# Optimization experiments

Measured on AMD Instinct MI355X. Metric: run time of the kernel, lower is better.

## Reference

```python
import jax, jax.numpy as jnp
import numpy as np
from jax import lax

B, T, U, V = 8, 160, 80, 512
BLANK = 0
FASTEMIT_LAMBDA = 0.0


def setup_inputs() -> dict:
    key = jax.random.key(0)
    k1, k2, k3, k4 = jax.random.split(key, 4)
    acts = jax.random.normal(k1, (B, T, U + 1, V), dtype=jnp.float32)
    labels = jax.random.randint(k2, (B, U), 1, V, dtype=jnp.int32)
    act_lens = jax.random.randint(k3, (B,), T // 2, T + 1, dtype=jnp.int32)
    label_lens = jax.random.randint(k4, (B,), U // 2, U + 1, dtype=jnp.int32)
    return {"acts": acts, "labels": labels, "act_lens": act_lens, "label_lens": label_lens}


def _alpha(blank_lp, label_lp):
    """Forward DP over the (T, U+1) lattice for one sample.
    blank_lp: [T, U+1] log P(blank | t, u);  label_lp: [T, U] log P(y_{u+1} | t, u).
    alpha[t, u] = logaddexp(alpha[t-1, u] + blank_lp[t-1, u], alpha[t, u-1] + label_lp[t, u-1]).
    """
    # row t=0: only label emissions -> prefix sums
    row0 = jnp.concatenate([jnp.zeros((1,), blank_lp.dtype), jnp.cumsum(label_lp[0])])

    def t_step(prev_row, xs):
        blank_prev, lab = xs                 # blank_lp[t-1]: [U+1], label_lp[t]: [U]
        base = prev_row + blank_prev         # come-from-below term, all u

        def u_step(carry, bl):
            b, l = bl
            new = jnp.logaddexp(b, carry + l)  # come-from-left recurrence along u
            return new, new

        _, rest = lax.scan(u_step, base[0], (base[1:], lab))
        row = jnp.concatenate([base[:1], rest])
        return row, row

    _, rows = lax.scan(t_step, row0, (blank_lp[:-1], label_lp[1:]))
    return jnp.concatenate([row0[None], rows], axis=0)  # [T, U+1]


def _rnnt_loss(acts, labels, act_lens, label_lens, blank=BLANK, fastemit_lambda=FASTEMIT_LAMBDA):
    lp = jax.nn.log_softmax(acts, axis=-1)                 # [B, T, U+1, V]
    blank_lp = lp[..., blank]                              # [B, T, U+1]
    # gather log-prob of emitting labels[u] at grid cell (t, u), u < U
    label_lp = jnp.take_along_axis(lp[:, :, :-1, :], labels[:, None, :, None], axis=-1)[..., 0]  # [B, T, U]
    alpha = jax.vmap(_alpha)(blank_lp, label_lp)           # [B, T, U+1]
    b_idx = jnp.arange(acts.shape[0])
    t_idx = act_lens - 1
    ll = alpha[b_idx, t_idx, label_lens] + blank_lp[b_idx, t_idx, label_lens]
    return -(1.0 + fastemit_lambda) * ll                   # [B]


def reference(acts, labels, act_lens, label_lens):
    return _rnnt_loss(acts, labels, act_lens, label_lens)
```

## Files before the change

kernel.cpp:

```cpp
#include <hip/hip_runtime.h>
#include <math.h>

#define RB 8
#define RT 160
#define RU 80
#define RV 512
#define UP1 81

#define L2E  1.44269504f
#define LN2  0.69314718f
#define NEGB (-1e30f)

__device__ __forceinline__ float fexp2(float x) { return __builtin_amdgcn_exp2f(x); }
__device__ __forceinline__ float flog2(float x) { return __builtin_amdgcn_logf(x); }

__device__ __forceinline__ float laE(float a, float b) {
    float m = fmaxf(a, b);
    float d = fminf(a, b) - m;
    return m + LN2 * flog2(1.0f + fexp2(d * L2E));
}

template<int CTRL, int RM>
__device__ __forceinline__ float dppf(float oldv, float src) {
    return __int_as_float(__builtin_amdgcn_update_dpp(
        __float_as_int(oldv), __float_as_int(src), CTRL, RM, 0xF, false));
}

__global__ __launch_bounds__(256) void lse_kernel(
    const float* __restrict__ acts, const int* __restrict__ labels,
    float* __restrict__ blank_lp, float* __restrict__ label_lp)
{
    const int wave = threadIdx.x >> 6;
    const int lane = threadIdx.x & 63;
    const int cell = blockIdx.x * 4 + wave;

    const int b   = cell / (RT * UP1);
    const int rem = cell - b * (RT * UP1);
    const int t   = rem / UP1;
    const int u   = rem - t * UP1;

    const float* p = acts + (size_t)cell * RV + lane * 8;
    const float4 v0 = *(const float4*)p;
    const float4 v1 = *(const float4*)(p + 4);

    float s = ((fexp2(v0.x * L2E) + fexp2(v0.y * L2E))
             + (fexp2(v0.z * L2E) + fexp2(v0.w * L2E)))
            + ((fexp2(v1.x * L2E) + fexp2(v1.y * L2E))
             + (fexp2(v1.z * L2E) + fexp2(v1.w * L2E)));

    s += dppf<0xB1,  0xF>(0.f, s);
    s += dppf<0x4E,  0xF>(0.f, s);
    s += dppf<0x141, 0xF>(0.f, s);
    s += dppf<0x140, 0xF>(0.f, s);
    s += dppf<0x142, 0xA>(0.f, s);
    s += dppf<0x143, 0xC>(0.f, s);

    const float lse = flog2(s) * LN2;
    const float blank_logit =
        __int_as_float(__builtin_amdgcn_readlane(__float_as_int(v0.x), 0));

    if (lane == 63) blank_lp[(b * RT + t) * UP1 + u] = blank_logit - lse;
    if (lane == 62 && u < RU) {
        const int lab = labels[b * RU + u];
        label_lp[(b * RT + t) * RU + u] = acts[(size_t)cell * RV + lab] - lse;
    }
}

__global__ __launch_bounds__(64) void dp_kernel(
    const float* __restrict__ blank_lp,
    const float* __restrict__ label_lp,
    const int* __restrict__ act_lens, const int* __restrict__ label_lens,
    float* __restrict__ out)
{
    const int b    = blockIdx.x;
    const int lane = threadIdx.x;
    const int u0   = lane * 2;
    const int u1   = lane * 2 + 1;
    const bool val0 = (u0 <= RU);
    const bool val1 = (u1 <= RU);

    const int t_idx = act_lens[b] - 1;
    const int ulen  = label_lens[b];

    const float* Bb = blank_lp + (size_t)b * RT * UP1;
    const float* Lb = label_lp + (size_t)b * RT * RU;

    float res  = 0.0f;
    bool  have = false;

    auto scanrow = [&](float b0_, float l0_, float b1_, float l1_,
                       float& N0, float& N1) {
        float cB = laE(b1_, l1_ + b0_);
        float cL = l1_ + l0_;
        { float oB = dppf<0x111,0xF>(NEGB,cB), oL = dppf<0x111,0xF>(0.f,cL);
          cB = laE(cB, cL + oB); cL += oL; }
        { float oB = dppf<0x112,0xF>(NEGB,cB), oL = dppf<0x112,0xF>(0.f,cL);
          cB = laE(cB, cL + oB); cL += oL; }
        { float oB = dppf<0x114,0xF>(NEGB,cB), oL = dppf<0x114,0xF>(0.f,cL);
          cB = laE(cB, cL + oB); cL += oL; }
        { float oB = dppf<0x118,0xF>(NEGB,cB), oL = dppf<0x118,0xF>(0.f,cL);
          cB = laE(cB, cL + oB); cL += oL; }
        float b15B = dppf<0x142,0xA>(NEGB,cB), b15L = dppf<0x142,0xA>(0.f,cL);
        cB = laE(cB, cL + b15B); cL += b15L;
        float b31B = dppf<0x143,0xC>(NEGB,cB), b31L = dppf<0x143,0xC>(0.f,cL);
        cB = laE(cB, cL + b31B); cL += b31L;
        float pB = dppf<0x111,0xF>(NEGB, cB);
        if      (lane == 16) pB = b15B;
        else if (lane == 32) pB = b31B;
        else if (lane == 48) pB = laE(b15B, b15L + b31B);
        N0 = laE(b0_, l0_ + pB);
        N1 = cB;
    };

    float prev0, prev1;
    {
        float b0_ = (u0 == 0) ? 0.0f : NEGB;
        float b1_ = NEGB;
        float l0_ = (u0 == 0) ? NEGB : (val0 ? Lb[u0 - 1] : 0.0f);
        float l1_ = val1 ? Lb[u1 - 1] : 0.0f;
        float N0, N1;
        scanrow(b0_, l0_, b1_, l1_, N0, N1);
        prev0 = val0 ? N0 : NEGB;
        prev1 = val1 ? N1 : NEGB;
        if (t_idx == 0) {
            if (ulen == u0)      { res = -(N0 + Bb[u0]); have = true; }
            else if (ulen == u1) { res = -(N1 + Bb[u1]); have = true; }
        }
    }

    float bp0 = val0 ? Bb[u0] : 0.0f;
    float bp1 = val1 ? Bb[u1] : 0.0f;
    float la0 = (val0 && u0 >= 1) ? Lb[RU + u0 - 1] : 0.0f;
    float la1 = val1 ? Lb[RU + u1 - 1] : 0.0f;

    for (int t = 1; t < RT; ++t) {
        float nbp0 = 0.f, nbp1 = 0.f, nla0 = 0.f, nla1 = 0.f;
        if (t + 1 < RT) {
            nbp0 = val0 ? Bb[t * UP1 + u0] : 0.0f;
            nbp1 = val1 ? Bb[t * UP1 + u1] : 0.0f;
            nla0 = (val0 && u0 >= 1) ? Lb[(t + 1) * RU + u0 - 1] : 0.0f;
            nla1 = val1 ? Lb[(t + 1) * RU + u1 - 1] : 0.0f;
        }

        float b0_ = val0 ? (prev0 + bp0) : NEGB;
        float b1_ = val1 ? (prev1 + bp1) : NEGB;
        float l0_ = (u0 == 0) ? NEGB : (val0 ? la0 : 0.0f);
        float l1_ = val1 ? la1 : 0.0f;

        float N0, N1;
        scanrow(b0_, l0_, b1_, l1_, N0, N1);
        prev0 = val0 ? N0 : NEGB;
        prev1 = val1 ? N1 : NEGB;

        if (t == t_idx) {
            if (ulen == u0)      { res = -(N0 + Bb[t * UP1 + u0]); have = true; }
            else if (ulen == u1) { res = -(N1 + Bb[t * UP1 + u1]); have = true; }
        }

        bp0 = nbp0; bp1 = nbp1; la0 = nla0; la1 = nla1;
    }

    if (have) out[b] = res;
}

extern "C" void kernel_launch(void* const* d_in, const int* in_sizes, int n_in,
                              void* d_out, int out_size, void* d_ws, size_t ws_size,
                              hipStream_t stream) {
    const float* acts       = (const float*)d_in[0];
    const int*   labels     = (const int*)d_in[1];
    const int*   act_lens   = (const int*)d_in[2];
    const int*   label_lens = (const int*)d_in[3];
    float* out = (float*)d_out;

    float* blank_lp = (float*)d_ws;
    float* label_lp = blank_lp + RB * RT * UP1;

    const int cells = RB * RT * UP1;
    lse_kernel<<<cells / 4, 256, 0, stream>>>(acts, labels, blank_lp, label_lp);
    dp_kernel<<<RB, 64, 0, stream>>>(blank_lp, label_lp, act_lens, label_lens, out);
}
```

Before: 398.0 us.

## Stage DP inputs in LDS and reformulate row scan as prefix-sum plus log-sum-exp scan

```diff
diff --git a/kernel.cpp b/kernel.cpp
--- a/kernel.cpp
+++ b/kernel.cpp
@@ -6,6 +6,7 @@
 #define RU 80
 #define RV 512
 #define UP1 81
+#define LSTR 84
 
 #define L2E  1.44269504f
 #define LN2  0.69314718f
@@ -66,98 +67,108 @@
     }
 }
 
-__global__ __launch_bounds__(64) void dp_kernel(
+__global__ __launch_bounds__(256) void dp_kernel(
     const float* __restrict__ blank_lp,
     const float* __restrict__ label_lp,
     const int* __restrict__ act_lens, const int* __restrict__ label_lens,
     float* __restrict__ out)
 {
-    const int b    = blockIdx.x;
-    const int lane = threadIdx.x;
-    const int u0   = lane * 2;
-    const int u1   = lane * 2 + 1;
-    const bool val0 = (u0 <= RU);
-    const bool val1 = (u1 <= RU);
+    extern __shared__ float smem[];
+    float* sB = smem;
+    float* sL = smem + RT * LSTR;
 
+    const int b   = blockIdx.x;
+    const int tid = threadIdx.x;
+
+    for (int i = tid; i < RT * LSTR; i += 256) { sB[i] = NEGB; sL[i] = 0.f; }
+    __syncthreads();
+    {
+        const float* gB = blank_lp + (size_t)b * RT * UP1;
+        for (int i = tid; i < RT * UP1; i += 256) {
+            int t = i / UP1, u = i - t * UP1;
+            sB[t * LSTR + u] = gB[i];
+        }
+        const float* gL = label_lp + (size_t)b * RT * RU;
+        for (int i = tid; i < RT * RU; i += 256) {
+            int t = i / RU, u = i - t * RU;
+            sL[t * LSTR + u + 1] = gL[i];
+        }
+    }
+    __syncthreads();
+    if (tid >= 64) return;
+
+    const int lane = tid;
+    const int u0 = 2 * lane, u1 = u0 + 1;
+    const int off = (u0 < 82) ? u0 : 82;
     const int t_idx = act_lens[b] - 1;
     const int ulen  = label_lens[b];
 
-    const float* Bb = blank_lp + (size_t)b * RT * UP1;
-    const float* Lb = label_lp + (size_t)b * RT * RU;
+    auto rdB = [&](int t) { return *(const float2*)&sB[t * LSTR + off]; };
+    auto rdL = [&](int t) { return *(const float2*)&sL[t * LSTR + off]; };
+
+    auto addscan = [&](float s) {
+        s += dppf<0x111, 0xF>(0.f, s);
+        s += dppf<0x112, 0xF>(0.f, s);
+        s += dppf<0x114, 0xF>(0.f, s);
+        s += dppf<0x118, 0xF>(0.f, s);
+        s += dppf<0x142, 0xA>(0.f, s);
+        s += dppf<0x143, 0xC>(0.f, s);
+        return s;
+    };
+    auto lsescan = [&](float v, float& excl) {
+        v = laE(v, dppf<0x111, 0xF>(NEGB, v));
+        v = laE(v, dppf<0x112, 0xF>(NEGB, v));
+        v = laE(v, dppf<0x114, 0xF>(NEGB, v));
+        v = laE(v, dppf<0x118, 0xF>(NEGB, v));
+        float t15 = dppf<0x142, 0xA>(NEGB, v); v = laE(v, t15);
+        float t31 = dppf<0x143, 0xC>(NEGB, v); v = laE(v, t31);
+        float p = dppf<0x111, 0xF>(NEGB, v);
+        p = (lane == 16) ? t15 : p;
+        p = (lane == 32) ? t31 : p;
+        p = (lane == 48) ? laE(t15, t31) : p;
+        excl = p;
+        return v;
+    };
 
     float res  = 0.0f;
     bool  have = false;
 
-    auto scanrow = [&](float b0_, float l0_, float b1_, float l1_,
-                       float& N0, float& N1) {
-        float cB = laE(b1_, l1_ + b0_);
-        float cL = l1_ + l0_;
-        { float oB = dppf<0x111,0xF>(NEGB,cB), oL = dppf<0x111,0xF>(0.f,cL);
-          cB = laE(cB, cL + oB); cL += oL; }
-        { float oB = dppf<0x112,0xF>(NEGB,cB), oL = dppf<0x112,0xF>(0.f,cL);
-          cB = laE(cB, cL + oB); cL += oL; }
-        { float oB = dppf<0x114,0xF>(NEGB,cB), oL = dppf<0x114,0xF>(0.f,cL);
-          cB = laE(cB, cL + oB); cL += oL; }
-        { float oB = dppf<0x118,0xF>(NEGB,cB), oL = dppf<0x118,0xF>(0.f,cL);
-          cB = laE(cB, cL + oB); cL += oL; }
-        float b15B = dppf<0x142,0xA>(NEGB,cB), b15L = dppf<0x142,0xA>(0.f,cL);
-        cB = laE(cB, cL + b15B); cL += b15L;
-        float b31B = dppf<0x143,0xC>(NEGB,cB), b31L = dppf<0x143,0xC>(0.f,cL);
-        cB = laE(cB, cL + b31B); cL += b31L;
-        float pB = dppf<0x111,0xF>(NEGB, cB);
-        if      (lane == 16) pB = b15B;
-        else if (lane == 32) pB = b31B;
-        else if (lane == 48) pB = laE(b15B, b15L + b31B);
-        N0 = laE(b0_, l0_ + pB);
-        N1 = cB;
-    };
-
     float prev0, prev1;
     {
-        float b0_ = (u0 == 0) ? 0.0f : NEGB;
-        float b1_ = NEGB;
-        float l0_ = (u0 == 0) ? NEGB : (val0 ? Lb[u0 - 1] : 0.0f);
-        float l1_ = val1 ? Lb[u1 - 1] : 0.0f;
-        float N0, N1;
-        scanrow(b0_, l0_, b1_, l1_, N0, N1);
-        prev0 = val0 ? N0 : NEGB;
-        prev1 = val1 ? N1 : NEGB;
-        if (t_idx == 0) {
-            if (ulen == u0)      { res = -(N0 + Bb[u0]); have = true; }
-            else if (ulen == u1) { res = -(N1 + Bb[u1]); have = true; }
-        }
+        float2 e = rdL(0);
+        float T = addscan(e.x + e.y);
+        prev1 = T;
+        prev0 = T - e.y;
     }
-
-    float bp0 = val0 ? Bb[u0] : 0.0f;
-    float bp1 = val1 ? Bb[u1] : 0.0f;
-    float la0 = (val0 && u0 >= 1) ? Lb[RU + u0 - 1] : 0.0f;
-    float la1 = val1 ? Lb[RU + u1 - 1] : 0.0f;
+    float2 bp = rdB(0);
+    if (t_idx == 0) {
+        if (ulen == u0)      { res = -(prev0 + bp.x); have = true; }
+        else if (ulen == u1) { res = -(prev1 + bp.y); have = true; }
+    }
+    float2 en = rdL(1);
 
     for (int t = 1; t < RT; ++t) {
-        float nbp0 = 0.f, nbp1 = 0.f, nla0 = 0.f, nla1 = 0.f;
-        if (t + 1 < RT) {
-            nbp0 = val0 ? Bb[t * UP1 + u0] : 0.0f;
-            nbp1 = val1 ? Bb[t * UP1 + u1] : 0.0f;
-            nla0 = (val0 && u0 >= 1) ? Lb[(t + 1) * RU + u0 - 1] : 0.0f;
-            nla1 = val1 ? Lb[(t + 1) * RU + u1 - 1] : 0.0f;
-        }
+        const float2 e_c  = en;
+        const float2 bp_c = bp;
+        const int tn = (t + 1 < RT) ? t + 1 : RT - 1;
+        en = rdL(tn);
+        bp = rdB(t);
 
-        float b0_ = val0 ? (prev0 + bp0) : NEGB;
-        float b1_ = val1 ? (prev1 + bp1) : NEGB;
-        float l0_ = (u0 == 0) ? NEGB : (val0 ? la0 : 0.0f);
-        float l1_ = val1 ? la1 : 0.0f;
-
-        float N0, N1;
-        scanrow(b0_, l0_, b1_, l1_, N0, N1);
-        prev0 = val0 ? N0 : NEGB;
-        prev1 = val1 ? N1 : NEGB;
+        const float T  = addscan(e_c.x + e_c.y);
+        const float Q1 = T, Q0 = T - e_c.y;
+        const float c0 = prev0 + bp_c.x - Q0;
+        const float c1 = prev1 + bp_c.y - Q1;
+        float excl;
+        const float V  = lsescan(laE(c0, c1), excl);
+        const float S1 = V;
+        const float S0 = laE(c0, excl);
+        prev0 = Q0 + S0;
+        prev1 = Q1 + S1;
 
         if (t == t_idx) {
-            if (ulen == u0)      { res = -(N0 + Bb[t * UP1 + u0]); have = true; }
-            else if (ulen == u1) { res = -(N1 + Bb[t * UP1 + u1]); have = true; }
+            if (ulen == u0)      { res = -(prev0 + bp.x); have = true; }
+            else if (ulen == u1) { res = -(prev1 + bp.y); have = true; }
         }
-
-        bp0 = nbp0; bp1 = nbp1; la0 = nla0; la1 = nla1;
     }
 
     if (have) out[b] = res;
@@ -177,5 +188,8 @@
 
     const int cells = RB * RT * UP1;
     lse_kernel<<<cells / 4, 256, 0, stream>>>(acts, labels, blank_lp, label_lp);
-    dp_kernel<<<RB, 64, 0, stream>>>(blank_lp, label_lp, act_lens, label_lens, out);
+
+    const size_t lds_bytes = 2u * RT * LSTR * sizeof(float);
+    dp_kernel<<<RB, 256, lds_bytes, stream>>>(blank_lp, label_lp,
+                                              act_lens, label_lens, out);
 }
```

New measurement: 344.0 us. 1.16x faster.
